# Kernel optimization log

Measured on AMD Instinct MI355X. Metric: run time of the kernel, lower is better.

## Reference

```python
import jax, jax.numpy as jnp
import numpy as np


def setup_inputs() -> dict:
    key = jax.random.key(0)
    ks = jax.random.split(key, 6)
    B, S, H, I, E, V = 8, 512, 512, 2048, 16, 32000
    std = 0.02
    return {
        "hidden_states": jax.random.normal(ks[0], (B, S, H), dtype=jnp.float32),
        "expert_probs": jax.random.uniform(ks[1], (B, E), dtype=jnp.float32),
        "Wg": jax.random.normal(ks[2], (E, I, H), dtype=jnp.float32) * std,
        "Wu": jax.random.normal(ks[3], (E, I, H), dtype=jnp.float32) * std,
        "Wd": jax.random.normal(ks[4], (E, H, I), dtype=jnp.float32) * (std * 0.5),
        "Wout": jax.random.normal(ks[5], (V, H), dtype=jnp.float32) * std,
        "top_k": 2,
    }


def reference(hidden_states, expert_probs, Wg, Wu, Wd, Wout, top_k):
    # Per-sample top-k routing (routing is over the batch dim, not tokens).
    topk_probs, topk_ids = jax.lax.top_k(expert_probs, top_k)  # (B, k)
    topk_probs = topk_probs / (jnp.sum(topk_probs, axis=-1, keepdims=True) + 1e-8)

    B, S, H = hidden_states.shape
    combined = jnp.zeros((B, S, H), dtype=hidden_states.dtype)
    for k in range(top_k):  # top_k is a small static int (2)
        eid = topk_ids[:, k]                     # (B,)
        wg = Wg[eid]                             # (B, I, H) gathered expert weights
        wu = Wu[eid]                             # (B, I, H)
        wd = Wd[eid]                             # (B, H, I)
        gate = jax.nn.silu(jnp.einsum('bsh,bih->bsi', hidden_states, wg))
        up = jnp.einsum('bsh,bih->bsi', hidden_states, wu)
        out = jnp.einsum('bsi,bhi->bsh', gate * up, wd)
        combined = combined + topk_probs[:, k][:, None, None] * out

    # Shared output projection -> logits (B, S, V)
    return jnp.einsum('bsh,vh->bsv', combined, Wout)
```

## Files before the change

### kernel.cpp

```cpp
#include <hip/hip_runtime.h>
#include <hip/hip_bf16.h>
#include <cstdint>

typedef __attribute__((ext_vector_type(8))) short bf16x8;
typedef __attribute__((ext_vector_type(4))) float f32x4;

#define MFMA16(a, b, c) __builtin_amdgcn_mfma_f32_16x16x32_bf16((a), (b), (c), 0, 0, 0)

__device__ __forceinline__ ushort f2bf(float x) {
  union { float f; uint32_t u; } c; c.f = x;
  uint32_t r = (c.u + 0x7FFFu + ((c.u >> 16) & 1u)) >> 16;
  return (ushort)r;
}

__device__ __forceinline__ void gload_lds16(const ushort* g, ushort* l) {
  __builtin_amdgcn_global_load_lds((__attribute__((address_space(1))) void*)g,
                                   (__attribute__((address_space(3))) void*)l, 16, 0, 0);
}

template <int NW, int INSTR>
__device__ __forceinline__ void stageT(const ushort* __restrict__ tileBase, int ld,
                                       ushort* lds, int wid, int lane) {
#pragma unroll
  for (int q = 0; q < INSTR; q++) {
    int r = (wid * INSTR + q) * 8 + (lane >> 3);
    int cb = ((lane & 7) * 16) ^ ((r & 7) << 4);
    gload_lds16(tileBase + (long)r * ld + (cb >> 1), lds + (wid * INSTR + q) * 512);
  }
}

__device__ __forceinline__ bf16x8 frag_read(const ushort* lds, int r, int kb) {
  int off = r * 128 + (kb ^ ((r & 7) << 4));
  return *(const bf16x8*)((const char*)lds + off);
}

template <int INSTR>
__device__ __forceinline__ void stage32(const ushort* __restrict__ tileBase, int ld,
                                        ushort* lds, int wid, int lane) {
#pragma unroll
  for (int q = 0; q < INSTR; q++) {
    int r = (wid * INSTR + q) * 16 + (lane >> 2);
    int cb = ((lane & 3) ^ ((r >> 1) & 3)) * 16;
    gload_lds16(tileBase + (long)r * ld + (cb >> 1), lds + (wid * INSTR + q) * 512);
  }
}

__device__ __forceinline__ bf16x8 frag_read32(const ushort* lds, int r, int kslot) {
  int off = r * 64 + ((kslot ^ ((r >> 1) & 3)) * 16);
  return *(const bf16x8*)((const char*)lds + off);
}

__device__ __forceinline__ bf16x8 pack8(float4 a, float4 b) {
  bf16x8 v;
  v[0] = (short)f2bf(a.x); v[1] = (short)f2bf(a.y);
  v[2] = (short)f2bf(a.z); v[3] = (short)f2bf(a.w);
  v[4] = (short)f2bf(b.x); v[5] = (short)f2bf(b.y);
  v[6] = (short)f2bf(b.z); v[7] = (short)f2bf(b.w);
  return v;
}

__device__ __forceinline__ void top2(const float* __restrict__ p, int& i0, int& i1,
                                     float& p0, float& p1) {
  float v0 = -1e30f, v1 = -1e30f; i0 = 0; i1 = 0;
#pragma unroll
  for (int e = 0; e < 16; e++) {
    float v = p[e];
    if (v > v0) { v1 = v0; i1 = i0; v0 = v; i0 = e; }
    else if (v > v1) { v1 = v; i1 = e; }
  }
  float s = 1.0f / (v0 + v1 + 1e-8f);
  p0 = v0 * s; p1 = v1 * s;
}

__global__ void cvt_hw(const float* __restrict__ hidden, const float* __restrict__ wout,
                       ushort* __restrict__ h_bf, ushort* __restrict__ wo_bf) {
  const long h4 = 2097152L / 4, w4 = 16384000L / 4, n4 = h4 + w4;
  long stride = (long)gridDim.x * blockDim.x;
  for (long g = (long)blockIdx.x * blockDim.x + threadIdx.x; g < n4; g += stride) {
    const float* src; ushort* dst; long o;
    if (g < h4) { src = hidden; dst = h_bf; o = g; }
    else { src = wout; dst = wo_bf; o = g - h4; }
    float4 v = ((const float4*)src)[o];
    ((ushort4*)dst)[o] = make_ushort4(f2bf(v.x), f2bf(v.y), f2bf(v.z), f2bf(v.w));
  }
}

__global__ __launch_bounds__(256, 3) void gateup128(
    const ushort* __restrict__ Hb, const float* __restrict__ Wgf,
    const float* __restrict__ Wuf, const float* __restrict__ eprobs,
    ushort* __restrict__ G) {
  constexpr int Hd = 512, I = 2048, S = 512, NTT = 16;
  __shared__ ushort As[2][128 * 32], B1s[2][64 * 32], B2s[2][64 * 32];

  int wg = blockIdx.x;
  int swz = (wg & 7) * 256 + (wg >> 3);
  int p = swz >> 7;
  int r7 = swz & 127;
  int rowT = r7 & 3, colT = r7 >> 2;
  const int b = p >> 1;
  int i0, i1; float q0, q1;
  top2(eprobs + b * 16, i0, i1, q0, q1);
  const int eid = (p & 1) ? i1 : i0;
  const int row0 = rowT * 128, col0 = colT * 64;
  const ushort* Ab  = Hb + ((long)b * S + row0) * Hd;
  const float*  B1f = Wgf + ((long)eid * I + col0) * Hd;
  const float*  B2f = Wuf + ((long)eid * I + col0) * Hd;

  const int tid = threadIdx.x, wid = tid >> 6, lane = tid & 63;
  const int wr = wid >> 1, wc = wid & 1;
  const int l15 = lane & 15;
  const int kslot = lane >> 4;
  const int rB = tid >> 2, sB = tid & 3;

  f32x4 acc1[4][2] = {};
  f32x4 acc2[4][2] = {};
  float4 b1a, b1b, b2a, b2b;

  auto ldB = [&](int t) {
    const float* p1 = B1f + (long)rB * Hd + t * 32 + sB * 8;
    const float* p2 = B2f + (long)rB * Hd + t * 32 + sB * 8;
    b1a = *(const float4*)p1; b1b = *(const float4*)(p1 + 4);
    b2a = *(const float4*)p2; b2b = *(const float4*)(p2 + 4);
  };
  auto wrB = [&](int buf) {
    int off = rB * 64 + ((sB ^ ((rB >> 1) & 3)) * 16);
    *(bf16x8*)((char*)B1s[buf] + off) = pack8(b1a, b1b);
    *(bf16x8*)((char*)B2s[buf] + off) = pack8(b2a, b2b);
  };

  ldB(0);
  stage32<2>(Ab, Hd, As[0], wid, lane);
  asm volatile("s_waitcnt vmcnt(2)" ::: "memory");
  wrB(0);
  ldB(1);
  asm volatile("s_waitcnt lgkmcnt(0)" ::: "memory");
  __builtin_amdgcn_sched_barrier(0);

  for (int t = 0; t < NTT; t++) {
    if (t + 1 < NTT) {
      stage32<2>(Ab + (t + 1) * 32, Hd, As[(t + 1) & 1], wid, lane);
      asm volatile("s_waitcnt vmcnt(10)" ::: "memory");
    } else {
      asm volatile("s_waitcnt vmcnt(0)" ::: "memory");
    }
    __builtin_amdgcn_s_barrier();
    __builtin_amdgcn_sched_barrier(0);
    const ushort* as = As[t & 1];
    bf16x8 av[4], bv[2];
#pragma unroll
    for (int i = 0; i < 4; i++) av[i] = frag_read32(as, wr * 64 + i * 16 + l15, kslot);
#pragma unroll
    for (int j = 0; j < 2; j++) bv[j] = frag_read32(B1s[t & 1], wc * 32 + j * 16 + l15, kslot);
    __builtin_amdgcn_s_setprio(1);
#pragma unroll
    for (int i = 0; i < 4; i++)
#pragma unroll
      for (int j = 0; j < 2; j++) acc1[i][j] = MFMA16(av[i], bv[j], acc1[i][j]);
    __builtin_amdgcn_s_setprio(0);
#pragma unroll
    for (int j = 0; j < 2; j++) bv[j] = frag_read32(B2s[t & 1], wc * 32 + j * 16 + l15, kslot);
    __builtin_amdgcn_s_setprio(1);
#pragma unroll
    for (int i = 0; i < 4; i++)
#pragma unroll
      for (int j = 0; j < 2; j++) acc2[i][j] = MFMA16(av[i], bv[j], acc2[i][j]);
    __builtin_amdgcn_s_setprio(0);
    if (t + 1 < NTT) {
      asm volatile("s_waitcnt vmcnt(2)" ::: "memory");
      wrB((t + 1) & 1);
      if (t + 2 < NTT) ldB(t + 2);
    }
    asm volatile("s_waitcnt lgkmcnt(0)" ::: "memory");
    __builtin_amdgcn_sched_barrier(0);
    __builtin_amdgcn_s_barrier();
  }

  ushort* Gout = G + (long)p * S * I;
#pragma unroll
  for (int i = 0; i < 4; i++) {
    int r = row0 + wr * 64 + i * 16 + ((lane >> 4) * 4);
#pragma unroll
    for (int j = 0; j < 2; j++) {
      int c = col0 + wc * 32 + j * 16 + l15;
#pragma unroll
      for (int q = 0; q < 4; q++) {
        float g = acc1[i][j][q], u = acc2[i][j][q];
        float sg = g / (1.0f + __expf(-g));
        Gout[(long)(r + q) * I + c] = f2bf(sg * u);
      }
    }
  }
}

__global__ __launch_bounds__(256) void down_fused(
    const ushort* __restrict__ G, const float* __restrict__ Wdf,
    const float* __restrict__ eprobs, ushort* __restrict__ Cb) {
  constexpr int I = 2048, Hd = 512, S = 512, NT = 64;
  const int b = blockIdx.z;
  const int row0 = blockIdx.x * 128, col0 = blockIdx.y * 32;
  __shared__ ushort As[2][128 * 64], Bs[2][32 * 64];
  const int tid = threadIdx.x, wid = tid >> 6, lane = tid & 63;
  int e0, e1; float p0, p1;
  top2(eprobs + b * 16, e0, e1, p0, p1);
  const ushort* A0 = G + ((long)(2 * b) * S + row0) * I;
  const ushort* A1 = G + ((long)(2 * b + 1) * S + row0) * I;
  const int rB = tid >> 3, sB = tid & 7;

  f32x4 acc[2][2] = {};
  float4 bda, bdb;

  auto stA = [&](int t2, int buf) {
    const ushort* An = (t2 < 32 ? A0 + t2 * 64 : A1 + (t2 - 32) * 64);
    stageT<4, 4>(An, I, As[buf], wid, lane);
  };
  auto ldB = [&](int t2) {
    int e = (t2 < 32) ? e0 : e1;
    const float* pb = Wdf + ((long)e * Hd + col0 + rB) * I + (t2 & 31) * 64 + sB * 8;
    bda = *(const float4*)pb; bdb = *(const float4*)(pb + 4);
  };
  auto wrB = [&](int buf) {
    int off = rB * 128 + ((sB * 16) ^ ((rB & 7) << 4));
    *(bf16x8*)((char*)Bs[buf] + off) = pack8(bda, bdb);
  };

  ldB(0);
  stA(0, 0);
  asm volatile("s_waitcnt vmcnt(4)" ::: "memory");
  wrB(0);
  ldB(1);
  asm volatile("s_waitcnt lgkmcnt(0)" ::: "memory");
  __builtin_amdgcn_sched_barrier(0);

  for (int t = 0; t < NT; t++) {
    if (t + 1 < NT) {
      stA(t + 1, (t + 1) & 1);
      asm volatile("s_waitcnt vmcnt(6)" ::: "memory");
    } else {
      asm volatile("s_waitcnt vmcnt(0)" ::: "memory");
    }
    __builtin_amdgcn_s_barrier();
    __builtin_amdgcn_sched_barrier(0);
    if (t == 32) {
      float ratio = p0 / p1;
#pragma unroll
      for (int i = 0; i < 2; i++)
#pragma unroll
        for (int j = 0; j < 2; j++) acc[i][j] *= ratio;
    }
#pragma unroll
    for (int ks = 0; ks < 2; ks++) {
      const int kb = ks * 64 + ((lane >> 4) * 16);
      bf16x8 av[2], bv[2];
#pragma unroll
      for (int i = 0; i < 2; i++) av[i] = frag_read(As[t & 1], wid * 32 + i * 16 + (lane & 15), kb);
#pragma unroll
      for (int j = 0; j < 2; j++) bv[j] = frag_read(Bs[t & 1], j * 16 + (lane & 15), kb);
      __builtin_amdgcn_s_setprio(1);
#pragma unroll
      for (int i = 0; i < 2; i++)
#pragma unroll
        for (int j = 0; j < 2; j++) acc[i][j] = MFMA16(av[i], bv[j], acc[i][j]);
      __builtin_amdgcn_s_setprio(0);
    }
    if (t + 1 < NT) {
      asm volatile("s_waitcnt vmcnt(4)" ::: "memory");
      wrB((t + 1) & 1);
      if (t + 2 < NT) ldB(t + 2);
    }
    asm volatile("s_waitcnt lgkmcnt(0)" ::: "memory");
    __builtin_amdgcn_sched_barrier(0);
    __builtin_amdgcn_s_barrier();
  }

  ushort* Co = Cb + ((long)b * S + row0) * Hd + col0;
#pragma unroll
  for (int i = 0; i < 2; i++) {
    int r = wid * 32 + i * 16 + ((lane >> 4) * 4);
#pragma unroll
    for (int j = 0; j < 2; j++) {
      int c = j * 16 + (lane & 15);
#pragma unroll
      for (int q = 0; q < 4; q++)
        Co[(long)(r + q) * Hd + c] = f2bf(p1 * acc[i][j][q]);
    }
  }
}

__global__ __launch_bounds__(256, 4) void gemm128_final(
    const ushort* __restrict__ A,
    const ushort* __restrict__ B,
    float* __restrict__ Out) {
  constexpr int K = 512, NTT = 16, LDC = 32000;
  __shared__ ushort As[2][128 * 32], Bs[2][128 * 32];

  int wg = blockIdx.x;
  int swz = (wg & 7) * 1000 + (wg >> 3);
  const int colT = swz / 32, rowT = swz % 32;
  const int row0 = rowT * 128, col0 = colT * 128;

  const int tid = threadIdx.x, wid = tid >> 6, lane = tid & 63;
  const int wr = wid >> 1, wc = wid & 1;
  const int l15 = lane & 15;
  const int kslot = lane >> 4;

  const ushort* Ab = A + (long)row0 * K;
  const ushort* Bb = B + (long)col0 * K;
  f32x4 acc[4][4] = {};

  stage32<2>(Ab, K, As[0], wid, lane);
  stage32<2>(Bb, K, Bs[0], wid, lane);

  for (int t = 0; t < NTT; t++) {
    if (t + 1 < NTT) {
      stage32<2>(Ab + (t + 1) * 32, K, As[(t + 1) & 1], wid, lane);
      stage32<2>(Bb + (t + 1) * 32, K, Bs[(t + 1) & 1], wid, lane);
      asm volatile("s_waitcnt vmcnt(4)" ::: "memory");
    } else {
      asm volatile("s_waitcnt vmcnt(0)" ::: "memory");
    }
    __builtin_amdgcn_s_barrier();
    __builtin_amdgcn_sched_barrier(0);
    const ushort* as = As[t & 1];
    const ushort* bs = Bs[t & 1];
    bf16x8 av[4], bv[4];
#pragma unroll
    for (int i = 0; i < 4; i++) av[i] = frag_read32(as, wr * 64 + i * 16 + l15, kslot);
#pragma unroll
    for (int j = 0; j < 4; j++) bv[j] = frag_read32(bs, wc * 64 + j * 16 + l15, kslot);
    __builtin_amdgcn_s_setprio(1);
#pragma unroll
    for (int i = 0; i < 4; i++)
#pragma unroll
      for (int j = 0; j < 4; j++)
        acc[i][j] = MFMA16(av[i], bv[j], acc[i][j]);
    __builtin_amdgcn_s_setprio(0);
    asm volatile("s_waitcnt lgkmcnt(0)" ::: "memory");
    __builtin_amdgcn_sched_barrier(0);
    __builtin_amdgcn_s_barrier();
  }

#pragma unroll
  for (int i = 0; i < 4; i++) {
    int r = row0 + wr * 64 + i * 16 + ((lane >> 4) * 4);
#pragma unroll
    for (int j = 0; j < 4; j++) {
      int c = col0 + wc * 64 + j * 16 + l15;
#pragma unroll
      for (int q = 0; q < 4; q++)
        __builtin_nontemporal_store(acc[i][j][q], &Out[(long)(r + q) * LDC + c]);
    }
  }
}

extern "C" void kernel_launch(void* const* d_in, const int* in_sizes, int n_in,
                              void* d_out, int out_size, void* d_ws, size_t ws_size,
                              hipStream_t stream) {
  const float* hidden = (const float*)d_in[0];
  const float* eprobs = (const float*)d_in[1];
  const float* Wg     = (const float*)d_in[2];
  const float* Wu     = (const float*)d_in[3];
  const float* Wd     = (const float*)d_in[4];
  const float* Wout   = (const float*)d_in[5];
  float* out = (float*)d_out;

  char* ws = (char*)d_ws;
  ushort* h_bf  = (ushort*)(ws + 256);
  ushort* wo_bf = h_bf  + 2097152L;
  ushort* Gbuf  = wo_bf + 16384000L;
  ushort* Cb    = Gbuf  + 16777216L;

  hipLaunchKernelGGL(cvt_hw, dim3(2048), dim3(256), 0, stream, hidden, Wout, h_bf, wo_bf);
  hipLaunchKernelGGL(gateup128, dim3(2048), dim3(256), 0, stream,
                     h_bf, Wg, Wu, eprobs, Gbuf);
  hipLaunchKernelGGL(down_fused, dim3(4, 16, 8), dim3(256), 0, stream,
                     Gbuf, Wd, eprobs, Cb);
  hipLaunchKernelGGL(gemm128_final, dim3(8000), dim3(256), 0, stream, Cb, wo_bf, out);
}
```

Baseline: 328.4 us.

## Fuse Wout fp32-to-bf16 conversion into final GEMM B-tile staging

Removes the separate pass that converted the 32000x512 Wout matrix to bf16. The final logits GEMM now loads fp32 Wout tiles into registers, packs them to bf16 and writes them into swizzled LDS, with a register prefetch one tile ahead. This saves a full read and write of the bf16 copy, but each of the 32 row-tile blocks now re-reads fp32 Wout (twice the bytes) and converts it again, adding VALU work inside the main loop.

```diff
diff --git a/kernel.cpp b/kernel.cpp
--- a/kernel.cpp
+++ b/kernel.cpp
@@ -72,16 +72,12 @@
   p0 = v0 * s; p1 = v1 * s;
 }
 
-__global__ void cvt_hw(const float* __restrict__ hidden, const float* __restrict__ wout,
-                       ushort* __restrict__ h_bf, ushort* __restrict__ wo_bf) {
-  const long h4 = 2097152L / 4, w4 = 16384000L / 4, n4 = h4 + w4;
+__global__ void cvt_h(const float* __restrict__ hidden, ushort* __restrict__ h_bf) {
+  const long n4 = 2097152L / 4;
   long stride = (long)gridDim.x * blockDim.x;
   for (long g = (long)blockIdx.x * blockDim.x + threadIdx.x; g < n4; g += stride) {
-    const float* src; ushort* dst; long o;
-    if (g < h4) { src = hidden; dst = h_bf; o = g; }
-    else { src = wout; dst = wo_bf; o = g - h4; }
-    float4 v = ((const float4*)src)[o];
-    ((ushort4*)dst)[o] = make_ushort4(f2bf(v.x), f2bf(v.y), f2bf(v.z), f2bf(v.w));
+    float4 v = ((const float4*)hidden)[g];
+    ((ushort4*)h_bf)[g] = make_ushort4(f2bf(v.x), f2bf(v.y), f2bf(v.z), f2bf(v.w));
   }
 }
 
@@ -288,7 +284,7 @@
 
 __global__ __launch_bounds__(256, 4) void gemm128_final(
     const ushort* __restrict__ A,
-    const ushort* __restrict__ B,
+    const float*  __restrict__ W,
     float* __restrict__ Out) {
   constexpr int K = 512, NTT = 16, LDC = 32000;
   __shared__ ushort As[2][128 * 32], Bs[2][128 * 32];
@@ -302,19 +298,37 @@
   const int wr = wid >> 1, wc = wid & 1;
   const int l15 = lane & 15;
   const int kslot = lane >> 4;
+  const int rB = tid >> 1, sB = (tid & 1) * 2;
 
   const ushort* Ab = A + (long)row0 * K;
-  const ushort* Bb = B + (long)col0 * K;
+  const float*  Wb = W + (long)col0 * K;
   f32x4 acc[4][4] = {};
-
+  float4 w0, w1, w2, w3;
+
+  auto ldB = [&](int t) {
+    const float* pb = Wb + (long)rB * K + t * 32 + sB * 8;
+    w0 = *(const float4*)pb;      w1 = *(const float4*)(pb + 4);
+    w2 = *(const float4*)(pb + 8); w3 = *(const float4*)(pb + 12);
+  };
+  auto wrB = [&](int buf) {
+    int o0 = rB * 64 + (((sB + 0) ^ ((rB >> 1) & 3)) * 16);
+    int o1 = rB * 64 + (((sB + 1) ^ ((rB >> 1) & 3)) * 16);
+    *(bf16x8*)((char*)Bs[buf] + o0) = pack8(w0, w1);
+    *(bf16x8*)((char*)Bs[buf] + o1) = pack8(w2, w3);
+  };
+
+  ldB(0);
   stage32<2>(Ab, K, As[0], wid, lane);
-  stage32<2>(Bb, K, Bs[0], wid, lane);
+  asm volatile("s_waitcnt vmcnt(2)" ::: "memory");
+  wrB(0);
+  ldB(1);
+  asm volatile("s_waitcnt lgkmcnt(0)" ::: "memory");
+  __builtin_amdgcn_sched_barrier(0);
 
   for (int t = 0; t < NTT; t++) {
     if (t + 1 < NTT) {
       stage32<2>(Ab + (t + 1) * 32, K, As[(t + 1) & 1], wid, lane);
-      stage32<2>(Bb + (t + 1) * 32, K, Bs[(t + 1) & 1], wid, lane);
-      asm volatile("s_waitcnt vmcnt(4)" ::: "memory");
+      asm volatile("s_waitcnt vmcnt(6)" ::: "memory");
     } else {
       asm volatile("s_waitcnt vmcnt(0)" ::: "memory");
     }
@@ -334,6 +348,11 @@
       for (int j = 0; j < 4; j++)
         acc[i][j] = MFMA16(av[i], bv[j], acc[i][j]);
     __builtin_amdgcn_s_setprio(0);
+    if (t + 1 < NTT) {
+      asm volatile("s_waitcnt vmcnt(2)" ::: "memory");
+      wrB((t + 1) & 1);
+      if (t + 2 < NTT) ldB(t + 2);
+    }
     asm volatile("s_waitcnt lgkmcnt(0)" ::: "memory");
     __builtin_amdgcn_sched_barrier(0);
     __builtin_amdgcn_s_barrier();
@@ -365,14 +384,13 @@
 
   char* ws = (char*)d_ws;
   ushort* h_bf  = (ushort*)(ws + 256);
-  ushort* wo_bf = h_bf  + 2097152L;
-  ushort* Gbuf  = wo_bf + 16384000L;
-  ushort* Cb    = Gbuf  + 16777216L;
-
-  hipLaunchKernelGGL(cvt_hw, dim3(2048), dim3(256), 0, stream, hidden, Wout, h_bf, wo_bf);
+  ushort* Gbuf  = h_bf + 2097152L;
+  ushort* Cb    = Gbuf + 16777216L;
+
+  hipLaunchKernelGGL(cvt_h, dim3(512), dim3(256), 0, stream, hidden, h_bf);
   hipLaunchKernelGGL(gateup128, dim3(2048), dim3(256), 0, stream,
                      h_bf, Wg, Wu, eprobs, Gbuf);
   hipLaunchKernelGGL(down_fused, dim3(4, 16, 8), dim3(256), 0, stream,
                      Gbuf, Wd, eprobs, Cb);
-  hipLaunchKernelGGL(gemm128_final, dim3(8000), dim3(256), 0, stream, Cb, wo_bf, out);
-}
+  hipLaunchKernelGGL(gemm128_final, dim3(8000), dim3(256), 0, stream, Cb, Wout, out);
+}
```

Result: slower. 443.5 us (+35.1%).

## Fuse hidden and Wout bf16 conversion into gate/up kernel, drop cvt_hw

Applied to the files above, without the earlier changes.

Removes the standalone conversion kernel. The gate/up GEMM now reads fp32 hidden states directly and converts them to bf16 in registers before writing LDS. Each block also converts a 2000-float4 slice of Wout to bf16 in its epilogue, so the 2048 blocks cover the whole matrix. This saves a launch and a separate pass over hidden, but adds more fp32 A-tile traffic and VGPRs to the gate/up loop. It also replaces the async global-to-LDS loads with a full vmcnt(0) wait each iteration, which may weaken overlap.

```diff
diff --git a/kernel.cpp b/kernel.cpp
--- a/kernel.cpp
+++ b/kernel.cpp
@@ -72,23 +72,11 @@
   p0 = v0 * s; p1 = v1 * s;
 }
 
-__global__ void cvt_hw(const float* __restrict__ hidden, const float* __restrict__ wout,
-                       ushort* __restrict__ h_bf, ushort* __restrict__ wo_bf) {
-  const long h4 = 2097152L / 4, w4 = 16384000L / 4, n4 = h4 + w4;
-  long stride = (long)gridDim.x * blockDim.x;
-  for (long g = (long)blockIdx.x * blockDim.x + threadIdx.x; g < n4; g += stride) {
-    const float* src; ushort* dst; long o;
-    if (g < h4) { src = hidden; dst = h_bf; o = g; }
-    else { src = wout; dst = wo_bf; o = g - h4; }
-    float4 v = ((const float4*)src)[o];
-    ((ushort4*)dst)[o] = make_ushort4(f2bf(v.x), f2bf(v.y), f2bf(v.z), f2bf(v.w));
-  }
-}
-
 __global__ __launch_bounds__(256, 3) void gateup128(
-    const ushort* __restrict__ Hb, const float* __restrict__ Wgf,
+    const float* __restrict__ Hf, const float* __restrict__ Wgf,
     const float* __restrict__ Wuf, const float* __restrict__ eprobs,
-    ushort* __restrict__ G) {
+    ushort* __restrict__ G, const float* __restrict__ WoutF,
+    ushort* __restrict__ wo_bf) {
   constexpr int Hd = 512, I = 2048, S = 512, NTT = 16;
   __shared__ ushort As[2][128 * 32], B1s[2][64 * 32], B2s[2][64 * 32];
 
@@ -102,20 +90,33 @@
   top2(eprobs + b * 16, i0, i1, q0, q1);
   const int eid = (p & 1) ? i1 : i0;
   const int row0 = rowT * 128, col0 = colT * 64;
-  const ushort* Ab  = Hb + ((long)b * S + row0) * Hd;
-  const float*  B1f = Wgf + ((long)eid * I + col0) * Hd;
-  const float*  B2f = Wuf + ((long)eid * I + col0) * Hd;
+  const float* Af  = Hf  + ((long)b * S + row0) * Hd;
+  const float* B1f = Wgf + ((long)eid * I + col0) * Hd;
+  const float* B2f = Wuf + ((long)eid * I + col0) * Hd;
 
   const int tid = threadIdx.x, wid = tid >> 6, lane = tid & 63;
   const int wr = wid >> 1, wc = wid & 1;
   const int l15 = lane & 15;
   const int kslot = lane >> 4;
   const int rB = tid >> 2, sB = tid & 3;
+  const int rA = tid >> 1, sA = (tid & 1) * 2;
 
   f32x4 acc1[4][2] = {};
   f32x4 acc2[4][2] = {};
+  float4 aw0, aw1, aw2, aw3;
   float4 b1a, b1b, b2a, b2b;
 
+  auto ldA = [&](int t) {
+    const float* pa = Af + (long)rA * Hd + t * 32 + sA * 8;
+    aw0 = *(const float4*)pa;       aw1 = *(const float4*)(pa + 4);
+    aw2 = *(const float4*)(pa + 8); aw3 = *(const float4*)(pa + 12);
+  };
+  auto wrA = [&](int buf) {
+    int o0 = rA * 64 + (((sA + 0) ^ ((rA >> 1) & 3)) * 16);
+    int o1 = rA * 64 + (((sA + 1) ^ ((rA >> 1) & 3)) * 16);
+    *(bf16x8*)((char*)As[buf] + o0) = pack8(aw0, aw1);
+    *(bf16x8*)((char*)As[buf] + o1) = pack8(aw2, aw3);
+  };
   auto ldB = [&](int t) {
     const float* p1 = B1f + (long)rB * Hd + t * 32 + sB * 8;
     const float* p2 = B2f + (long)rB * Hd + t * 32 + sB * 8;
@@ -128,21 +129,14 @@
     *(bf16x8*)((char*)B2s[buf] + off) = pack8(b2a, b2b);
   };
 
-  ldB(0);
-  stage32<2>(Ab, Hd, As[0], wid, lane);
-  asm volatile("s_waitcnt vmcnt(2)" ::: "memory");
-  wrB(0);
-  ldB(1);
+  ldA(0); ldB(0);
+  asm volatile("s_waitcnt vmcnt(0)" ::: "memory");
+  wrA(0); wrB(0);
+  ldA(1); ldB(1);
   asm volatile("s_waitcnt lgkmcnt(0)" ::: "memory");
   __builtin_amdgcn_sched_barrier(0);
 
   for (int t = 0; t < NTT; t++) {
-    if (t + 1 < NTT) {
-      stage32<2>(Ab + (t + 1) * 32, Hd, As[(t + 1) & 1], wid, lane);
-      asm volatile("s_waitcnt vmcnt(10)" ::: "memory");
-    } else {
-      asm volatile("s_waitcnt vmcnt(0)" ::: "memory");
-    }
     __builtin_amdgcn_s_barrier();
     __builtin_amdgcn_sched_barrier(0);
     const ushort* as = As[t & 1];
@@ -166,9 +160,9 @@
       for (int j = 0; j < 2; j++) acc2[i][j] = MFMA16(av[i], bv[j], acc2[i][j]);
     __builtin_amdgcn_s_setprio(0);
     if (t + 1 < NTT) {
-      asm volatile("s_waitcnt vmcnt(2)" ::: "memory");
-      wrB((t + 1) & 1);
-      if (t + 2 < NTT) ldB(t + 2);
+      asm volatile("s_waitcnt vmcnt(0)" ::: "memory");
+      wrA((t + 1) & 1); wrB((t + 1) & 1);
+      if (t + 2 < NTT) { ldA(t + 2); ldB(t + 2); }
     }
     asm volatile("s_waitcnt lgkmcnt(0)" ::: "memory");
     __builtin_amdgcn_sched_barrier(0);
@@ -188,6 +182,15 @@
         float sg = g / (1.0f + __expf(-g));
         Gout[(long)(r + q) * I + c] = f2bf(sg * u);
       }
+    }
+  }
+
+  {
+    const float4* wsrc = (const float4*)WoutF + (long)blockIdx.x * 2000;
+    ushort4* wdst = (ushort4*)wo_bf + (long)blockIdx.x * 2000;
+    for (int idx = tid; idx < 2000; idx += 256) {
+      float4 v = wsrc[idx];
+      wdst[idx] = make_ushort4(f2bf(v.x), f2bf(v.y), f2bf(v.z), f2bf(v.w));
     }
   }
 }
@@ -364,14 +367,12 @@
   float* out = (float*)d_out;
 
   char* ws = (char*)d_ws;
-  ushort* h_bf  = (ushort*)(ws + 256);
-  ushort* wo_bf = h_bf  + 2097152L;
+  ushort* wo_bf = (ushort*)(ws + 256);
   ushort* Gbuf  = wo_bf + 16384000L;
-  ushort* Cb    = Gbuf  + 16777216L;
-
-  hipLaunchKernelGGL(cvt_hw, dim3(2048), dim3(256), 0, stream, hidden, Wout, h_bf, wo_bf);
+  ushort* Cb    = Gbuf + 16777216L;
+
   hipLaunchKernelGGL(gateup128, dim3(2048), dim3(256), 0, stream,
-                     h_bf, Wg, Wu, eprobs, Gbuf);
+                     hidden, Wg, Wu, eprobs, Gbuf, Wout, wo_bf);
   hipLaunchKernelGGL(down_fused, dim3(4, 16, 8), dim3(256), 0, stream,
                      Gbuf, Wd, eprobs, Cb);
   hipLaunchKernelGGL(gemm128_final, dim3(8000), dim3(256), 0, stream, Cb, wo_bf, out);
```

Result: slower. 343.8 us (+4.7%).
